# Kernel optimization log

Measured on AMD Instinct MI355X. Metric: run time of the kernel, lower is better.

## Reference

```python
import jax, jax.numpy as jnp
import numpy as np

N_NODES = 50000
N_EDGES = 800000
D = 128
N_LAYERS = 3
EPS = 1e-5  # torch LayerNorm default


def _gcn_conv(x, src, dst, dinv, W, b):
    # PyG GCNConv: h = x @ W; out[i] = sum_{(s->i)} dinv[s]*dinv[i]*h[s] + dinv[i]^2*h[i] + b
    h = x @ W
    norm = dinv[src] * dinv[dst]                      # [E]
    msgs = h[src] * norm[:, None]                     # [E, D] gather
    agg = jax.ops.segment_sum(msgs, dst, num_segments=N_NODES)  # scatter-add
    agg = agg + h * (dinv * dinv)[:, None]            # self-loop term
    return agg + b


def _layer_norm(x, gamma, beta):
    mu = jnp.mean(x, axis=-1, keepdims=True)
    var = jnp.mean(jnp.square(x - mu), axis=-1, keepdims=True)
    return (x - mu) * jax.lax.rsqrt(var + EPS) * gamma + beta


def setup_inputs() -> dict:
    key = jax.random.key(0)
    ks = jax.random.split(key, 4)
    x = jax.random.normal(ks[0], (N_NODES, D), dtype=jnp.float32)
    edge_index = jax.random.randint(ks[1], (2, N_EDGES), 0, N_NODES, dtype=jnp.int64)
    Ws = jax.random.normal(ks[2], (N_LAYERS, D, D), dtype=jnp.float32) * (1.0 / np.sqrt(D))
    bs = jnp.zeros((N_LAYERS, D), dtype=jnp.float32)
    gammas = jnp.ones((N_LAYERS, D), dtype=jnp.float32)
    betas = jnp.zeros((N_LAYERS, D), dtype=jnp.float32)
    return {"x": x, "edge_index": edge_index, "Ws": Ws, "bs": bs,
            "gammas": gammas, "betas": betas}


def reference(x, edge_index, Ws, bs, gammas, betas):
    src, dst = edge_index[0], edge_index[1]
    # GCN symmetric normalization with self-loops: deg[i] = in-degree(i) + 1
    deg = jnp.zeros((N_NODES,), dtype=x.dtype).at[dst].add(1.0) + 1.0
    dinv = jax.lax.rsqrt(deg)
    h = x
    for i in range(N_LAYERS):
        x_new = _gcn_conv(h, src, dst, dinv, Ws[i], bs[i])
        x_new = _layer_norm(x_new, gammas[i], betas[i])
        x_new = jax.nn.relu(x_new)  # dropout is identity in eval mode
        h = h + x_new if i > 0 else x_new
    return h
```

## Files before the change

kernel.cpp:

```cpp
#include <hip/hip_runtime.h>
#include <hip/hip_bf16.h>

#define NN 50000
#define NE 800000
#define DD 128
#define NB 196
#define NCH 8
#define CHSZ 6250
#define NC2 (NN * NCH)
#define NSB 391
#define PH (64 * NB)
#define FS 2048
#define NSL 391
#define HHB (NSL * 8)
#define QB 3125
#define WB 192
#define LN_EPS 1e-5f

typedef __bf16 bf16x8 __attribute__((ext_vector_type(8)));
typedef float f32x4 __attribute__((ext_vector_type(4)));

__device__ inline ushort f2bf_bits(float f) {
    union { __hip_bfloat16 h; ushort u; } c;
    c.h = __float2bfloat16(f);
    return c.u;
}

__device__ inline void accum_q(float* acc, uint2 qv, float ww) {
    uint lo = qv.x, hi = qv.y;
    acc[0] = fmaf(ww, (float)(char)(lo), acc[0]);
    acc[1] = fmaf(ww, (float)(char)(lo >> 8), acc[1]);
    acc[2] = fmaf(ww, (float)(char)(lo >> 16), acc[2]);
    acc[3] = fmaf(ww, (float)(char)(lo >> 24), acc[3]);
    acc[4] = fmaf(ww, (float)(char)(hi), acc[4]);
    acc[5] = fmaf(ww, (float)(char)(hi >> 8), acc[5]);
    acc[6] = fmaf(ww, (float)(char)(hi >> 16), acc[6]);
    acc[7] = fmaf(ww, (float)(char)(hi >> 24), acc[7]);
}

__global__ void hist_cast_kernel(const int* __restrict__ src, const int* __restrict__ dst,
                                 int* __restrict__ counts2, int* __restrict__ rank,
                                 const float* __restrict__ x, uint2* __restrict__ qf0,
                                 float* __restrict__ sc0, const float* __restrict__ W,
                                 ushort* __restrict__ Wt) {
    int b = blockIdx.x;
    if (b < HHB) {
        int slice = b >> 3;
        int r = b & 7;
        int base = slice * FS;
#pragma unroll 2
        for (int i = threadIdx.x; i < FS; i += 256) {
            int e = base + i;
            if (e < NE) {
                int d = dst[e];
                if (d / CHSZ == r) {
                    int s = src[e];
                    rank[e] = atomicAdd(&counts2[d * NCH + s / CHSZ], 1);
                }
            }
        }
    } else if (b < HHB + QB) {
        int bb = b - HHB;
        int group = threadIdx.x >> 4, t = threadIdx.x & 15;
        int node = bb * 16 + group;
        const float4* xr = (const float4*)(x + (size_t)node * DD + t * 8);
        float4 v0 = xr[0], v1 = xr[1];
        float vals[8] = {v0.x, v0.y, v0.z, v0.w, v1.x, v1.y, v1.z, v1.w};
        float am = 0.f;
#pragma unroll
        for (int i = 0; i < 8; ++i) am = fmaxf(am, fabsf(vals[i]));
#pragma unroll
        for (int off = 1; off <= 8; off <<= 1) am = fmaxf(am, __shfl_xor(am, off, 64));
        float inv = 127.f / fmaxf(am, 1e-20f);
        uint lo = 0, hi = 0;
#pragma unroll
        for (int i = 0; i < 4; ++i) {
            int q = __float2int_rn(vals[i] * inv);
            lo |= ((uint)(q & 0xff)) << (8 * i);
        }
#pragma unroll
        for (int i = 0; i < 4; ++i) {
            int q = __float2int_rn(vals[4 + i] * inv);
            hi |= ((uint)(q & 0xff)) << (8 * i);
        }
        uint2 pk; pk.x = lo; pk.y = hi;
        qf0[node * 16 + t] = pk;
        if (t == 0) sc0[node] = am / 127.f;
    } else {
        int i = (b - HHB - QB) * 256 + threadIdx.x;
        int l = i >> 14, k = (i >> 7) & 127, n = i & 127;
        Wt[l * 16384 + n * 128 + k] = f2bf_bits(W[i]);
    }
}

__global__ __launch_bounds__(1024) void scan1024_blocks(int* __restrict__ data,
                                                        int* __restrict__ bsums) {
    __shared__ int ws[16];
    int gid = blockIdx.x * 1024 + threadIdx.x;
    int lane = threadIdx.x & 63, wid = threadIdx.x >> 6;
    int v = (gid < NC2) ? data[gid] : 0;
    int x = v;
#pragma unroll
    for (int off = 1; off < 64; off <<= 1) {
        int t = __shfl_up(x, off, 64);
        if (lane >= off) x += t;
    }
    if (lane == 63) ws[wid] = x;
    __syncthreads();
    if (threadIdx.x == 0) {
        int run = 0;
        for (int i = 0; i < 16; ++i) { int t = ws[i]; ws[i] = run; run += t; }
        bsums[blockIdx.x] = run;
    }
    __syncthreads();
    if (gid < NC2) data[gid] = x - v + ws[wid];
}

__global__ __launch_bounds__(1024) void scan_sums1024(int* __restrict__ bsums, int nb) {
    __shared__ int ws[16];
    int tid = threadIdx.x;
    int lane = tid & 63, wid = tid >> 6;
    int v = (tid < nb) ? bsums[tid] : 0;
    int x = v;
#pragma unroll
    for (int off = 1; off < 64; off <<= 1) {
        int t = __shfl_up(x, off, 64);
        if (lane >= off) x += t;
    }
    if (lane == 63) ws[wid] = x;
    __syncthreads();
    if (tid == 0) {
        int run = 0;
        for (int i = 0; i < 16; ++i) { int t = ws[i]; ws[i] = run; run += t; }
    }
    __syncthreads();
    if (tid < nb) bsums[tid] = x - v + ws[wid];
}

__global__ void finalize_kernel(const int* __restrict__ excl2, const int* __restrict__ bsums,
                                int* __restrict__ row_ptr, float* __restrict__ dinv,
                                int* __restrict__ degarr, int* __restrict__ bh) {
    __shared__ int lh[64];
    if (threadIdx.x < 64) lh[threadIdx.x] = 0;
    __syncthreads();
    int d = blockIdx.x * 256 + threadIdx.x;
    if (d < NN) {
        int base = d * NCH;
        int p0 = excl2[base] + bsums[base >> 10];
        int nxt = (d == NN - 1) ? NE : excl2[base + NCH] + bsums[(base + NCH) >> 10];
        int deg = nxt - p0;
        row_ptr[d] = p0;
        dinv[d] = rsqrtf((float)deg + 1.0f);
        degarr[d] = deg;
        atomicAdd(&lh[63 - min(deg, 63)], 1);
    }
    __syncthreads();
    if (threadIdx.x < 64) bh[threadIdx.x * NB + blockIdx.x] = lh[threadIdx.x];
    if (blockIdx.x == 0 && threadIdx.x == 0) row_ptr[NN] = NE;
}

__global__ __launch_bounds__(1024) void permscan_kernel(int* __restrict__ bh) {
    __shared__ int wsum[16];
    const int CH = 13;
    int tid = threadIdx.x;
    int base = tid * CH;
    int vals[CH];
    int s = 0;
#pragma unroll
    for (int i = 0; i < CH; ++i) {
        int idx = base + i;
        int v = (idx < PH) ? bh[idx] : 0;
        vals[i] = s;
        s += v;
    }
    int lane = tid & 63, wid = tid >> 6;
    int x = s;
#pragma unroll
    for (int off = 1; off < 64; off <<= 1) {
        int t = __shfl_up(x, off, 64);
        if (lane >= off) x += t;
    }
    if (lane == 63) wsum[wid] = x;
    __syncthreads();
    if (tid == 0) {
        int run = 0;
        for (int i = 0; i < 16; ++i) { int t = wsum[i]; wsum[i] = run; run += t; }
    }
    __syncthreads();
    int texcl = x - s + wsum[wid];
#pragma unroll
    for (int i = 0; i < CH; ++i) {
        int idx = base + i;
        if (idx < PH) bh[idx] = texcl + vals[i];
    }
}

__global__ void scatter_fill_kernel(const int* __restrict__ degarr, const int* __restrict__ bh,
                                    int* __restrict__ perm, const int* __restrict__ src,
                                    const int* __restrict__ dst, const int* __restrict__ excl2,
                                    const int* __restrict__ bsums, const int* __restrict__ rank,
                                    const float* __restrict__ dinv, int2* __restrict__ edge2) {
    if (blockIdx.x < NB) {
        __shared__ int lh[64];
        __shared__ int lbase[64];
        if (threadIdx.x < 64) {
            lh[threadIdx.x] = 0;
            lbase[threadIdx.x] = bh[threadIdx.x * NB + blockIdx.x];
        }
        __syncthreads();
        int gid = blockIdx.x * 256 + threadIdx.x;
        if (gid < NN) {
            int b = 63 - min(degarr[gid], 63);
            int r = atomicAdd(&lh[b], 1);
            perm[lbase[b] + r] = gid;
        }
    } else {
        int bb = blockIdx.x - NB;
        int slice = bb >> 3;
        int r = bb & 7;
        int base = slice * FS;
#pragma unroll 2
        for (int i = threadIdx.x; i < FS; i += 256) {
            int e = base + i;
            if (e < NE) {
                int d = dst[e];
                if (d / CHSZ == r) {
                    int s = src[e];
                    int bin = d * NCH + s / CHSZ;
                    int pos = excl2[bin] + bsums[bin >> 10] + rank[e];
                    int2 o;
                    o.x = s;
                    o.y = __float_as_int(dinv[s] * dinv[d]);
                    edge2[pos] = o;
                }
            }
        }
    }
}

template <bool RES, bool FINAL>
__global__ __launch_bounds__(256) void layer_kernel(
    const uint2* __restrict__ qin, const float* __restrict__ scin,
    const ushort* __restrict__ fin, const int* __restrict__ row_ptr,
    const int2* __restrict__ edge2, const int* __restrict__ perm,
    const float* __restrict__ dinv, const ushort* __restrict__ Wt,
    const float* __restrict__ bias, const float* __restrict__ gamma,
    const float* __restrict__ beta, ushort* __restrict__ fout, char* __restrict__ qfout,
    float* __restrict__ scout, float* __restrict__ out) {
    __shared__ uint4 sA[16 * 17];
    __shared__ int sNode[16];
    __shared__ float sLN1[4][16], sLN2[4][16];
    __shared__ float sMX[4][16];

    int w = threadIdx.x >> 6, lane = threadIdx.x & 63;
    int g = lane >> 4, t = lane & 15;
    int arow = w * 4 + g;
    int slot = blockIdx.x * 16 + arow;
    int node = perm[slot];
    if (t == 0) sNode[arow] = node;

    {
        int beg = row_ptr[node], end = row_ptr[node + 1];
        float acc[8] = {};
        int e = beg;
        for (; e + 8 <= end; e += 8) {
            int2 a[8];
            uint2 qv[8];
            float sc[8];
#pragma unroll
            for (int j = 0; j < 8; ++j) a[j] = edge2[e + j];
#pragma unroll
            for (int j = 0; j < 8; ++j) {
                qv[j] = qin[a[j].x * 16 + t];
                sc[j] = scin[a[j].x];
            }
#pragma unroll
            for (int j = 0; j < 8; ++j) accum_q(acc, qv[j], __int_as_float(a[j].y) * sc[j]);
        }
        for (; e + 4 <= end; e += 4) {
            int2 a[4];
            uint2 qv[4];
            float sc[4];
#pragma unroll
            for (int j = 0; j < 4; ++j) a[j] = edge2[e + j];
#pragma unroll
            for (int j = 0; j < 4; ++j) {
                qv[j] = qin[a[j].x * 16 + t];
                sc[j] = scin[a[j].x];
            }
#pragma unroll
            for (int j = 0; j < 4; ++j) accum_q(acc, qv[j], __int_as_float(a[j].y) * sc[j]);
        }
        for (; e < end; ++e) {
            int2 a = edge2[e];
            uint2 qv = qin[a.x * 16 + t];
            accum_q(acc, qv, __int_as_float(a.y) * scin[a.x]);
        }
        {
            float di = dinv[node];
            uint2 qv = qin[node * 16 + t];
            accum_q(acc, qv, di * di * scin[node]);
        }
        union { ushort us[8]; uint4 u; } pk;
#pragma unroll
        for (int i = 0; i < 8; ++i) pk.us[i] = f2bf_bits(acc[i]);
        sA[arow * 17 + t] = pk.u;
    }
    __syncthreads();

    int q = lane >> 4, m = lane & 15;
    f32x4 c0 = (f32x4){0.f, 0.f, 0.f, 0.f};
    f32x4 c1 = (f32x4){0.f, 0.f, 0.f, 0.f};
    int n0 = 16 * (2 * w), n1 = 16 * (2 * w + 1);
#pragma unroll
    for (int kk = 0; kk < 4; ++kk) {
        bf16x8 af = *(const bf16x8*)&sA[m * 17 + kk * 4 + q];
        bf16x8 b0 = *(const bf16x8*)(Wt + (n0 + m) * DD + kk * 32 + q * 8);
        bf16x8 b1 = *(const bf16x8*)(Wt + (n1 + m) * DD + kk * 32 + q * 8);
        c0 = __builtin_amdgcn_mfma_f32_16x16x32_bf16(af, b0, c0, 0, 0, 0);
        c1 = __builtin_amdgcn_mfma_f32_16x16x32_bf16(af, b1, c1, 0, 0, 0);
    }

    float bb0 = bias[n0 + m], bb1 = bias[n1 + m];
    float s1[4], s2[4];
#pragma unroll
    for (int r = 0; r < 4; ++r) {
        float v0 = c0[r] + bb0, v1 = c1[r] + bb1;
        c0[r] = v0; c1[r] = v1;
        s1[r] = v0 + v1;
        s2[r] = v0 * v0 + v1 * v1;
    }
#pragma unroll
    for (int off = 1; off <= 8; off <<= 1) {
#pragma unroll
        for (int r = 0; r < 4; ++r) {
            s1[r] += __shfl_xor(s1[r], off, 64);
            s2[r] += __shfl_xor(s2[r], off, 64);
        }
    }
    if (m == 0) {
#pragma unroll
        for (int r = 0; r < 4; ++r) {
            sLN1[w][q * 4 + r] = s1[r];
            sLN2[w][q * 4 + r] = s2[r];
        }
    }
    __syncthreads();
    float ga0 = gamma[n0 + m], ga1 = gamma[n1 + m];
    float be0 = beta[n0 + m], be1 = beta[n1 + m];
    float o0v[4], o1v[4], rmax[4];
#pragma unroll
    for (int r = 0; r < 4; ++r) {
        int row = q * 4 + r;
        float S1 = sLN1[0][row] + sLN1[1][row] + sLN1[2][row] + sLN1[3][row];
        float S2 = sLN2[0][row] + sLN2[1][row] + sLN2[2][row] + sLN2[3][row];
        float mu = S1 * (1.f / 128.f);
        float var = S2 * (1.f / 128.f) - mu * mu;
        float rstd = rsqrtf(var + LN_EPS);
        int nd = sNode[row];
        size_t rb = (size_t)nd * DD;
        float o0 = fmaxf((c0[r] - mu) * rstd * ga0 + be0, 0.f);
        float o1 = fmaxf((c1[r] - mu) * rstd * ga1 + be1, 0.f);
        if (RES) {
            o0 += __uint_as_float(((uint)fin[rb + n0 + m]) << 16);
            o1 += __uint_as_float(((uint)fin[rb + n1 + m]) << 16);
        }
        if (FINAL) {
            out[rb + n0 + m] = o0;
            out[rb + n1 + m] = o1;
        } else {
            fout[rb + n0 + m] = f2bf_bits(o0);
            fout[rb + n1 + m] = f2bf_bits(o1);
            o0v[r] = o0; o1v[r] = o1;
            rmax[r] = fmaxf(o0, o1);
        }
    }
    if (!FINAL) {
#pragma unroll
        for (int off = 1; off <= 8; off <<= 1) {
#pragma unroll
            for (int r = 0; r < 4; ++r) rmax[r] = fmaxf(rmax[r], __shfl_xor(rmax[r], off, 64));
        }
        if (m == 0) {
#pragma unroll
            for (int r = 0; r < 4; ++r) sMX[w][q * 4 + r] = rmax[r];
        }
        __syncthreads();
#pragma unroll
        for (int r = 0; r < 4; ++r) {
            int row = q * 4 + r;
            float M = fmaxf(fmaxf(sMX[0][row], sMX[1][row]), fmaxf(sMX[2][row], sMX[3][row]));
            float inv = 127.f / fmaxf(M, 1e-20f);
            int nd = sNode[row];
            if (w == 0 && m == 0) scout[nd] = M / 127.f;
            int q0 = min(__float2int_rn(o0v[r] * inv), 127);
            int q1 = min(__float2int_rn(o1v[r] * inv), 127);
            qfout[(size_t)nd * DD + n0 + m] = (char)q0;
            qfout[(size_t)nd * DD + n1 + m] = (char)q1;
        }
    }
}


extern "C" void kernel_launch(void* const* d_in, const int* in_sizes, int n_in,
                              void* d_out, int out_size, void* d_ws, size_t ws_size,
                              hipStream_t stream) {
    const float* x = (const float*)d_in[0];
    const int* edge = (const int*)d_in[1];
    const float* Ws = (const float*)d_in[2];
    const float* bs = (const float*)d_in[3];
    const float* gs = (const float*)d_in[4];
    const float* bes = (const float*)d_in[5];
    float* out = (float*)d_out;
    const int* src = edge;
    const int* dst = edge + NE;

    char* p = (char*)d_ws;
    int* counts2 = (int*)p;     p += (size_t)NC2 * 4;
    int* bsums = (int*)p;       p += 1024 * 4;
    int* row_ptr = (int*)p;     p += (size_t)(NN + 4) * 4;
    int* rank = (int*)p;        p += (size_t)NE * 4;
    float* dinv = (float*)p;    p += (size_t)NN * 4;
    int* degarr = (int*)p;      p += (size_t)NN * 4;
    int* bh = (int*)p;          p += (size_t)PH * 4;
    int* perm = (int*)p;        p += (size_t)NN * 4;
    int2* edge2 = (int2*)p;     p += (size_t)NE * 8;
    ushort* fb0 = (ushort*)p;   p += (size_t)NN * DD * 2;
    ushort* fb1 = (ushort*)p;   p += (size_t)NN * DD * 2;
    char* qf0 = (char*)p;       p += (size_t)NN * DD;
    char* qf1 = (char*)p;       p += (size_t)NN * DD;
    float* sc0 = (float*)p;     p += (size_t)NN * 4;
    float* sc1 = (float*)p;     p += (size_t)NN * 4;
    ushort* Wt = (ushort*)p;    p += (size_t)3 * DD * DD * 2;

    hipMemsetAsync(counts2, 0, (size_t)NC2 * 4, stream);
    hist_cast_kernel<<<HHB + QB + WB, 256, 0, stream>>>(src, dst, counts2, rank, x,
                                                        (uint2*)qf0, sc0, Ws, Wt);
    scan1024_blocks<<<NSB, 1024, 0, stream>>>(counts2, bsums);
    scan_sums1024<<<1, 1024, 0, stream>>>(bsums, NSB);
    finalize_kernel<<<NB, 256, 0, stream>>>(counts2, bsums, row_ptr, dinv, degarr, bh);
    permscan_kernel<<<1, 1024, 0, stream>>>(bh);
    scatter_fill_kernel<<<NB + NSL * 8, 256, 0, stream>>>(degarr, bh, perm, src, dst, counts2,
                                                          bsums, rank, dinv, edge2);

    int lg = NN / 16;
    layer_kernel<false, false><<<lg, 256, 0, stream>>>(
        (const uint2*)qf0, sc0, fb0, row_ptr, edge2, perm, dinv, Wt, bs, gs, bes,
        fb1, qf1, sc1, out);
    layer_kernel<true, false><<<lg, 256, 0, stream>>>(
        (const uint2*)qf1, sc1, fb1, row_ptr, edge2, perm, dinv, Wt + 16384, bs + DD, gs + DD,
        bes + DD, fb0, qf0, sc0, out);
    layer_kernel<true, true><<<lg, 256, 0, stream>>>(
        (const uint2*)qf0, sc0, fb0, row_ptr, edge2, perm, dinv, Wt + 32768, bs + 2 * DD,
        gs + 2 * DD, bes + 2 * DD, fb1, qf1, sc1, out);
}
```

Before: 284.0 us.

## Software-pipeline edge gather with double-buffered batches and padded edge tail

Rewrites the per-node neighbor aggregation loop as a two-stage software pipeline. Edge batches of eight are loaded one batch ahead, and feature gathers for the next batch are issued before the current batch is accumulated. Partial batches are handled by masking with zero weights, so the remainder loops go away. To keep the over-read of the final batch in bounds, the edge array is padded with eight zero entries. It also raises launch bounds to request four blocks per CU, which adds register pressure against the doubled buffers and may cause spills.

Result: slower. 386.9 us (+36.2%).

```diff
diff --git a/kernel.cpp b/kernel.cpp
--- a/kernel.cpp
+++ b/kernel.cpp
@@ -216,6 +216,10 @@
         }
     } else {
         int bb = blockIdx.x - NB;
+        if (bb == 0 && threadIdx.x < 8) {
+            int2 z; z.x = 0; z.y = 0;
+            edge2[NE + threadIdx.x] = z;
+        }
         int slice = bb >> 3;
         int r = bb & 7;
         int base = slice * FS;
@@ -239,7 +243,7 @@
 }
 
 template <bool RES, bool FINAL>
-__global__ __launch_bounds__(256) void layer_kernel(
+__global__ __launch_bounds__(256, 4) void layer_kernel(
     const uint2* __restrict__ qin, const float* __restrict__ scin,
     const ushort* __restrict__ fin, const int* __restrict__ row_ptr,
     const int2* __restrict__ edge2, const int* __restrict__ perm,
@@ -260,47 +264,55 @@
     if (t == 0) sNode[arow] = node;
 
     {
-        int beg = row_ptr[node], end = row_ptr[node + 1];
+        int beg = row_ptr[node];
+        int deg = row_ptr[node + 1] - beg;
+        int nb = (deg + 7) >> 3;
         float acc[8] = {};
-        int e = beg;
-        for (; e + 8 <= end; e += 8) {
-            int2 a[8];
-            uint2 qv[8];
-            float sc[8];
-#pragma unroll
-            for (int j = 0; j < 8; ++j) a[j] = edge2[e + j];
+
+        uint2 qself = qin[node * 16 + t];
+        float di = dinv[node];
+        float sself = scin[node];
+
+        const int2* ebase = edge2 + beg;
+        int2 A0[8], A1[8];
+        uint2 Q0[8], Q1[8];
+        float W0[8], W1[8];
+
+        auto LOADE = [&](int2* A, int b) {
+#pragma unroll
+            for (int j = 0; j < 8; ++j) A[j] = ebase[b * 8 + j];
+        };
+        auto ISSUE = [&](const int2* A, uint2* Q, float* Wv, int b) {
+            int lim = deg - b * 8;
 #pragma unroll
             for (int j = 0; j < 8; ++j) {
-                qv[j] = qin[a[j].x * 16 + t];
-                sc[j] = scin[a[j].x];
+                int s = (j < lim) ? A[j].x : A[0].x;
+                Q[j] = qin[s * 16 + t];
+                Wv[j] = (j < lim) ? __int_as_float(A[j].y) * scin[s] : 0.f;
             }
-#pragma unroll
-            for (int j = 0; j < 8; ++j) accum_q(acc, qv[j], __int_as_float(a[j].y) * sc[j]);
-        }
-        for (; e + 4 <= end; e += 4) {
-            int2 a[4];
-            uint2 qv[4];
-            float sc[4];
-#pragma unroll
-            for (int j = 0; j < 4; ++j) a[j] = edge2[e + j];
-#pragma unroll
-            for (int j = 0; j < 4; ++j) {
-                qv[j] = qin[a[j].x * 16 + t];
-                sc[j] = scin[a[j].x];
+        };
+        auto CONSUME = [&](const uint2* Q, const float* Wv) {
+#pragma unroll
+            for (int j = 0; j < 8; ++j) accum_q(acc, Q[j], Wv[j]);
+        };
+
+        if (nb > 0) {
+            LOADE(A0, 0);
+            if (nb > 1) LOADE(A1, 1);
+            ISSUE(A0, Q0, W0, 0);
+            int b = 0;
+            for (; b + 2 <= nb; b += 2) {
+                if (b + 2 < nb) LOADE(A0, b + 2);
+                ISSUE(A1, Q1, W1, b + 1);
+                CONSUME(Q0, W0);
+                if (b + 3 < nb) LOADE(A1, b + 3);
+                if (b + 2 < nb) ISSUE(A0, Q0, W0, b + 2);
+                CONSUME(Q1, W1);
             }
-#pragma unroll
-            for (int j = 0; j < 4; ++j) accum_q(acc, qv[j], __int_as_float(a[j].y) * sc[j]);
-        }
-        for (; e < end; ++e) {
-            int2 a = edge2[e];
-            uint2 qv = qin[a.x * 16 + t];
-            accum_q(acc, qv, __int_as_float(a.y) * scin[a.x]);
-        }
-        {
-            float di = dinv[node];
-            uint2 qv = qin[node * 16 + t];
-            accum_q(acc, qv, di * di * scin[node]);
-        }
+            if (b < nb) CONSUME(Q0, W0);
+        }
+        accum_q(acc, qself, di * di * sself);
+
         union { ushort us[8]; uint4 u; } pk;
 #pragma unroll
         for (int i = 0; i < 8; ++i) pk.us[i] = f2bf_bits(acc[i]);
@@ -424,7 +436,7 @@
     int* degarr = (int*)p;      p += (size_t)NN * 4;
     int* bh = (int*)p;          p += (size_t)PH * 4;
     int* perm = (int*)p;        p += (size_t)NN * 4;
-    int2* edge2 = (int2*)p;     p += (size_t)NE * 8;
+    int2* edge2 = (int2*)p;     p += (size_t)(NE + 8) * 8;
     ushort* fb0 = (ushort*)p;   p += (size_t)NN * DD * 2;
     ushort* fb1 = (ushort*)p;   p += (size_t)NN * DD * 2;
     char* qf0 = (char*)p;       p += (size_t)NN * DD;
```

## Split int8 feature gather into low/high halves across two kernels for cache fit

Applied to the files above, without the earlier changes.

The int8 node features are split into separate low-64 and high-64 channel arrays. A new agg_lo kernel aggregates the low half into a bf16 buffer, and the layer kernel aggregates the high half and loads the precomputed low half before the MFMA. The goal is to shrink the random-gather working set per kernel so it fits better in L2, while edge lists and row pointers are read twice. The edge loop is also restructured into padded fixed-8 batches using a zeroed tail, and nontemporal loads and stores are added for streaming data.

New measurement: 392.9 us. 1.38x slower.

```diff
diff --git a/kernel.cpp b/kernel.cpp
--- a/kernel.cpp
+++ b/kernel.cpp
@@ -19,6 +19,7 @@
 
 typedef __bf16 bf16x8 __attribute__((ext_vector_type(8)));
 typedef float f32x4 __attribute__((ext_vector_type(4)));
+typedef uint uv2 __attribute__((ext_vector_type(2)));
 
 __device__ inline ushort f2bf_bits(float f) {
     union { __hip_bfloat16 h; ushort u; } c;
@@ -26,23 +27,18 @@
     return c.u;
 }
 
-__device__ inline void accum_q(float* acc, uint2 qv, float ww) {
-    uint lo = qv.x, hi = qv.y;
-    acc[0] = fmaf(ww, (float)(char)(lo), acc[0]);
-    acc[1] = fmaf(ww, (float)(char)(lo >> 8), acc[1]);
-    acc[2] = fmaf(ww, (float)(char)(lo >> 16), acc[2]);
-    acc[3] = fmaf(ww, (float)(char)(lo >> 24), acc[3]);
-    acc[4] = fmaf(ww, (float)(char)(hi), acc[4]);
-    acc[5] = fmaf(ww, (float)(char)(hi >> 8), acc[5]);
-    acc[6] = fmaf(ww, (float)(char)(hi >> 16), acc[6]);
-    acc[7] = fmaf(ww, (float)(char)(hi >> 24), acc[7]);
+__device__ inline void accum_q4(float* acc, uint qv, float ww) {
+    acc[0] = fmaf(ww, (float)(char)(qv), acc[0]);
+    acc[1] = fmaf(ww, (float)(char)(qv >> 8), acc[1]);
+    acc[2] = fmaf(ww, (float)(char)(qv >> 16), acc[2]);
+    acc[3] = fmaf(ww, (float)(char)(qv >> 24), acc[3]);
 }
 
 __global__ void hist_cast_kernel(const int* __restrict__ src, const int* __restrict__ dst,
                                  int* __restrict__ counts2, int* __restrict__ rank,
-                                 const float* __restrict__ x, uint2* __restrict__ qf0,
-                                 float* __restrict__ sc0, const float* __restrict__ W,
-                                 ushort* __restrict__ Wt) {
+                                 const float* __restrict__ x, uint2* __restrict__ qlo0,
+                                 uint2* __restrict__ qhi0, float* __restrict__ sc0,
+                                 const float* __restrict__ W, ushort* __restrict__ Wt) {
     int b = blockIdx.x;
     if (b < HHB) {
         int slice = b >> 3;
@@ -84,7 +80,8 @@
             hi |= ((uint)(q & 0xff)) << (8 * i);
         }
         uint2 pk; pk.x = lo; pk.y = hi;
-        qf0[node * 16 + t] = pk;
+        if (t < 8) qlo0[node * 8 + t] = pk;
+        else       qhi0[node * 8 + (t - 8)] = pk;
         if (t == 0) sc0[node] = am / 127.f;
     } else {
         int i = (b - HHB - QB) * 256 + threadIdx.x;
@@ -216,6 +213,10 @@
         }
     } else {
         int bb = blockIdx.x - NB;
+        if (bb == 0 && threadIdx.x < 8) {
+            int2 z; z.x = 0; z.y = 0;
+            edge2[NE + threadIdx.x] = z;
+        }
         int slice = bb >> 3;
         int r = bb & 7;
         int base = slice * FS;
@@ -238,16 +239,57 @@
     }
 }
 
+__global__ __launch_bounds__(256) void agg_lo_kernel(
+    const uint* __restrict__ qlo, const float* __restrict__ scin,
+    const int* __restrict__ row_ptr, const int2* __restrict__ edge2,
+    const int* __restrict__ perm, const float* __restrict__ dinv,
+    uv2* __restrict__ Alo) {
+    int w = threadIdx.x >> 6, lane = threadIdx.x & 63;
+    int g = lane >> 4, t = lane & 15;
+    int slot = blockIdx.x * 16 + w * 4 + g;
+    int node = perm[slot];
+    int beg = row_ptr[node], deg = row_ptr[node + 1] - beg;
+    float acc[4] = {};
+    uint qself = qlo[node * 16 + t];
+    float di = dinv[node], cself = scin[node];
+    const long* eb = (const long*)(edge2 + beg);
+    int nbt = (deg + 7) >> 3;
+    for (int b = 0; b < nbt; ++b) {
+        int lim = deg - b * 8;
+        int As[8]; float Aw[8]; uint Q[8]; float Wv[8];
+#pragma unroll
+        for (int j = 0; j < 8; ++j) {
+            long av = __builtin_nontemporal_load(eb + b * 8 + j);
+            As[j] = (int)(uint)(av & 0xffffffffL);
+            Aw[j] = __int_as_float((int)(av >> 32));
+        }
+#pragma unroll
+        for (int j = 0; j < 8; ++j) {
+            int s = (j < lim) ? As[j] : As[0];
+            Q[j] = qlo[s * 16 + t];
+            Wv[j] = (j < lim) ? Aw[j] * scin[s] : 0.f;
+        }
+#pragma unroll
+        for (int j = 0; j < 8; ++j) accum_q4(acc, Q[j], Wv[j]);
+    }
+    accum_q4(acc, qself, di * di * cself);
+    union { ushort us[4]; uv2 u; } pk;
+#pragma unroll
+    for (int i = 0; i < 4; ++i) pk.us[i] = f2bf_bits(acc[i]);
+    __builtin_nontemporal_store(pk.u, Alo + (size_t)node * 16 + t);
+}
+
 template <bool RES, bool FINAL>
 __global__ __launch_bounds__(256) void layer_kernel(
-    const uint2* __restrict__ qin, const float* __restrict__ scin,
-    const ushort* __restrict__ fin, const int* __restrict__ row_ptr,
-    const int2* __restrict__ edge2, const int* __restrict__ perm,
-    const float* __restrict__ dinv, const ushort* __restrict__ Wt,
-    const float* __restrict__ bias, const float* __restrict__ gamma,
-    const float* __restrict__ beta, ushort* __restrict__ fout, char* __restrict__ qfout,
+    const uint* __restrict__ qhi, const float* __restrict__ scin,
+    const uv2* __restrict__ Alo, const ushort* __restrict__ fin,
+    const int* __restrict__ row_ptr, const int2* __restrict__ edge2,
+    const int* __restrict__ perm, const float* __restrict__ dinv,
+    const ushort* __restrict__ Wt, const float* __restrict__ bias,
+    const float* __restrict__ gamma, const float* __restrict__ beta,
+    ushort* __restrict__ fout, char* __restrict__ qlo_out, char* __restrict__ qhi_out,
     float* __restrict__ scout, float* __restrict__ out) {
-    __shared__ uint4 sA[16 * 17];
+    __shared__ uv2 sA2[16][34];
     __shared__ int sNode[16];
     __shared__ float sLN1[4][16], sLN2[4][16];
     __shared__ float sMX[4][16];
@@ -260,51 +302,38 @@
     if (t == 0) sNode[arow] = node;
 
     {
-        int beg = row_ptr[node], end = row_ptr[node + 1];
-        float acc[8] = {};
-        int e = beg;
-        for (; e + 8 <= end; e += 8) {
-            int2 a[8];
-            uint2 qv[8];
-            float sc[8];
-#pragma unroll
-            for (int j = 0; j < 8; ++j) a[j] = edge2[e + j];
+        int beg = row_ptr[node], deg = row_ptr[node + 1] - beg;
+        float acc[4] = {};
+        uint qself = qhi[node * 16 + t];
+        float di = dinv[node], cself = scin[node];
+        const long* eb = (const long*)(edge2 + beg);
+        int nbt = (deg + 7) >> 3;
+        for (int b = 0; b < nbt; ++b) {
+            int lim = deg - b * 8;
+            int As[8]; float Aw[8]; uint Q[8]; float Wv[8];
 #pragma unroll
             for (int j = 0; j < 8; ++j) {
-                qv[j] = qin[a[j].x * 16 + t];
-                sc[j] = scin[a[j].x];
+                long av = __builtin_nontemporal_load(eb + b * 8 + j);
+                As[j] = (int)(uint)(av & 0xffffffffL);
+                Aw[j] = __int_as_float((int)(av >> 32));
             }
 #pragma unroll
-            for (int j = 0; j < 8; ++j) accum_q(acc, qv[j], __int_as_float(a[j].y) * sc[j]);
-        }
-        for (; e + 4 <= end; e += 4) {
-            int2 a[4];
-            uint2 qv[4];
-            float sc[4];
-#pragma unroll
-            for (int j = 0; j < 4; ++j) a[j] = edge2[e + j];
-#pragma unroll
-            for (int j = 0; j < 4; ++j) {
-                qv[j] = qin[a[j].x * 16 + t];
-                sc[j] = scin[a[j].x];
+            for (int j = 0; j < 8; ++j) {
+                int s = (j < lim) ? As[j] : As[0];
+                Q[j] = qhi[s * 16 + t];
+                Wv[j] = (j < lim) ? Aw[j] * scin[s] : 0.f;
             }
 #pragma unroll
-            for (int j = 0; j < 4; ++j) accum_q(acc, qv[j], __int_as_float(a[j].y) * sc[j]);
-        }
-        for (; e < end; ++e) {
-            int2 a = edge2[e];
-            uint2 qv = qin[a.x * 16 + t];
-            accum_q(acc, qv, __int_as_float(a.y) * scin[a.x]);
-        }
-        {
-            float di = dinv[node];
-            uint2 qv = qin[node * 16 + t];
-            accum_q(acc, qv, di * di * scin[node]);
-        }
-        union { ushort us[8]; uint4 u; } pk;
-#pragma unroll
-        for (int i = 0; i < 8; ++i) pk.us[i] = f2bf_bits(acc[i]);
-        sA[arow * 17 + t] = pk.u;
+            for (int j = 0; j < 8; ++j) accum_q4(acc, Q[j], Wv[j]);
+        }
+        accum_q4(acc, qself, di * di * cself);
+
+        union { ushort us[4]; uv2 u; } pk;
+#pragma unroll
+        for (int i = 0; i < 4; ++i) pk.us[i] = f2bf_bits(acc[i]);
+        sA2[arow][16 + t] = pk.u;
+        uv2 loq = __builtin_nontemporal_load(Alo + (size_t)node * 16 + t);
+        sA2[arow][t] = loq;
     }
     __syncthreads();
 
@@ -314,7 +343,7 @@
     int n0 = 16 * (2 * w), n1 = 16 * (2 * w + 1);
 #pragma unroll
     for (int kk = 0; kk < 4; ++kk) {
-        bf16x8 af = *(const bf16x8*)&sA[m * 17 + kk * 4 + q];
+        bf16x8 af = *(const bf16x8*)((const char*)&sA2[0][0] + m * 272 + (kk * 4 + q) * 16);
         bf16x8 b0 = *(const bf16x8*)(Wt + (n0 + m) * DD + kk * 32 + q * 8);
         bf16x8 b1 = *(const bf16x8*)(Wt + (n1 + m) * DD + kk * 32 + q * 8);
         c0 = __builtin_amdgcn_mfma_f32_16x16x32_bf16(af, b0, c0, 0, 0, 0);
@@ -362,15 +391,15 @@
         float o0 = fmaxf((c0[r] - mu) * rstd * ga0 + be0, 0.f);
         float o1 = fmaxf((c1[r] - mu) * rstd * ga1 + be1, 0.f);
         if (RES) {
-            o0 += __uint_as_float(((uint)fin[rb + n0 + m]) << 16);
-            o1 += __uint_as_float(((uint)fin[rb + n1 + m]) << 16);
+            o0 += __uint_as_float(((uint)__builtin_nontemporal_load(&fin[rb + n0 + m])) << 16);
+            o1 += __uint_as_float(((uint)__builtin_nontemporal_load(&fin[rb + n1 + m])) << 16);
         }
         if (FINAL) {
-            out[rb + n0 + m] = o0;
-            out[rb + n1 + m] = o1;
+            __builtin_nontemporal_store(o0, &out[rb + n0 + m]);
+            __builtin_nontemporal_store(o1, &out[rb + n1 + m]);
         } else {
-            fout[rb + n0 + m] = f2bf_bits(o0);
-            fout[rb + n1 + m] = f2bf_bits(o1);
+            __builtin_nontemporal_store(f2bf_bits(o0), &fout[rb + n0 + m]);
+            __builtin_nontemporal_store(f2bf_bits(o1), &fout[rb + n1 + m]);
             o0v[r] = o0; o1v[r] = o1;
             rmax[r] = fmaxf(o0, o1);
         }
@@ -395,8 +424,13 @@
             if (w == 0 && m == 0) scout[nd] = M / 127.f;
             int q0 = min(__float2int_rn(o0v[r] * inv), 127);
             int q1 = min(__float2int_rn(o1v[r] * inv), 127);
-            qfout[(size_t)nd * DD + n0 + m] = (char)q0;
-            qfout[(size_t)nd * DD + n1 + m] = (char)q1;
+            if (n0 < 64) {
+                qlo_out[(size_t)nd * 64 + n0 + m] = (char)q0;
+                qlo_out[(size_t)nd * 64 + n1 + m] = (char)q1;
+            } else {
+                qhi_out[(size_t)nd * 64 + n0 - 64 + m] = (char)q0;
+                qhi_out[(size_t)nd * 64 + n1 - 64 + m] = (char)q1;
+            }
         }
     }
 }
@@ -424,18 +458,22 @@
     int* degarr = (int*)p;      p += (size_t)NN * 4;
     int* bh = (int*)p;          p += (size_t)PH * 4;
     int* perm = (int*)p;        p += (size_t)NN * 4;
-    int2* edge2 = (int2*)p;     p += (size_t)NE * 8;
+    int2* edge2 = (int2*)p;     p += (size_t)(NE + 8) * 8;
     ushort* fb0 = (ushort*)p;   p += (size_t)NN * DD * 2;
     ushort* fb1 = (ushort*)p;   p += (size_t)NN * DD * 2;
-    char* qf0 = (char*)p;       p += (size_t)NN * DD;
-    char* qf1 = (char*)p;       p += (size_t)NN * DD;
+    char* qlo0 = (char*)p;      p += (size_t)NN * 64;
+    char* qhi0 = (char*)p;      p += (size_t)NN * 64;
+    char* qlo1 = (char*)p;      p += (size_t)NN * 64;
+    char* qhi1 = (char*)p;      p += (size_t)NN * 64;
     float* sc0 = (float*)p;     p += (size_t)NN * 4;
     float* sc1 = (float*)p;     p += (size_t)NN * 4;
     ushort* Wt = (ushort*)p;    p += (size_t)3 * DD * DD * 2;
+    uv2* Alo = (uv2*)p;         p += (size_t)NN * 64 * 2;
 
     hipMemsetAsync(counts2, 0, (size_t)NC2 * 4, stream);
     hist_cast_kernel<<<HHB + QB + WB, 256, 0, stream>>>(src, dst, counts2, rank, x,
-                                                        (uint2*)qf0, sc0, Ws, Wt);
+                                                        (uint2*)qlo0, (uint2*)qhi0, sc0,
+                                                        Ws, Wt);
     scan1024_blocks<<<NSB, 1024, 0, stream>>>(counts2, bsums);
     scan_sums1024<<<1, 1024, 0, stream>>>(bsums, NSB);
     finalize_kernel<<<NB, 256, 0, stream>>>(counts2, bsums, row_ptr, dinv, degarr, bh);
@@ -444,13 +482,19 @@
                                                           bsums, rank, dinv, edge2);
 
     int lg = NN / 16;
+    agg_lo_kernel<<<lg, 256, 0, stream>>>((const uint*)qlo0, sc0, row_ptr, edge2, perm,
+                                          dinv, Alo);
     layer_kernel<false, false><<<lg, 256, 0, stream>>>(
-        (const uint2*)qf0, sc0, fb0, row_ptr, edge2, perm, dinv, Wt, bs, gs, bes,
-        fb1, qf1, sc1, out);
+        (const uint*)qhi0, sc0, Alo, fb0, row_ptr, edge2, perm, dinv, Wt, bs, gs, bes,
+        fb1, qlo1, qhi1, sc1, out);
+    agg_lo_kernel<<<lg, 256, 0, stream>>>((const uint*)qlo1, sc1, row_ptr, edge2, perm,
+                                          dinv, Alo);
     layer_kernel<true, false><<<lg, 256, 0, stream>>>(
-        (const uint2*)qf1, sc1, fb1, row_ptr, edge2, perm, dinv, Wt + 16384, bs + DD, gs + DD,
-        bes + DD, fb0, qf0, sc0, out);
+        (const uint*)qhi1, sc1, Alo, fb1, row_ptr, edge2, perm, dinv, Wt + 16384, bs + DD,
+        gs + DD, bes + DD, fb0, qlo0, qhi0, sc0, out);
+    agg_lo_kernel<<<lg, 256, 0, stream>>>((const uint*)qlo0, sc0, row_ptr, edge2, perm,
+                                          dinv, Alo);
     layer_kernel<true, true><<<lg, 256, 0, stream>>>(
-        (const uint2*)qf0, sc0, fb0, row_ptr, edge2, perm, dinv, Wt + 32768, bs + 2 * DD,
-        gs + 2 * DD, bes + 2 * DD, fb1, qf1, sc1, out);
-}
+        (const uint*)qhi0, sc0, Alo, fb0, row_ptr, edge2, perm, dinv, Wt + 32768, bs + 2 * DD,
+        gs + 2 * DD, bes + 2 * DD, fb1, qlo1, qhi1, sc1, out);
+}
```
